# Kernel tuning notes

Hardware: AMD Instinct MI355X
Metric: run time of the kernel (lower is better)

Reference implementation:

```python
import jax, jax.numpy as jnp
import numpy as np

B_GRAPHS = 16      # number of graphs in batch
NPG = 8192         # nodes per graph
N = B_GRAPHS * NPG # 131072 total nodes
F_DIM = 64         # node feature dim
K_CLUST = 16       # n_clusters
DEG = 32           # avg degree
E = N * DEG        # 4,194,304 edges


def setup_inputs() -> dict:
    key = jax.random.key(0)
    k1, k2, k3, k4, k5 = jax.random.split(key, 5)
    x = jax.random.normal(k1, (N, F_DIM), jnp.float32)
    W = jax.random.normal(k2, (F_DIM, K_CLUST), jnp.float32) / np.sqrt(F_DIM)
    b = jnp.zeros((K_CLUST,), jnp.float32)
    # edges constrained within each graph -> block-diagonal adjacency (PyG batching)
    g = jnp.repeat(jnp.arange(B_GRAPHS, dtype=jnp.int32), E // B_GRAPHS)
    edge_row = g * NPG + jax.random.randint(k3, (E,), 0, NPG, jnp.int32)
    edge_col = g * NPG + jax.random.randint(k4, (E,), 0, NPG, jnp.int32)
    edge_weight = jax.random.uniform(k5, (E,), jnp.float32)
    return {"x": x, "W": W, "b": b, "edge_weight": edge_weight,
            "edge_row": edge_row, "edge_col": edge_col, "num_graphs": B_GRAPHS}


def _forward(x, W, b, edge_weight, edge_row, edge_col, num_graphs):
    Ntot, Fd = x.shape
    K = W.shape[1]
    Bn = num_graphs
    n = Ntot // Bn  # equal-size graphs (ptr = n * arange(B+1))

    s = x @ W + b                                   # [N,K] cluster logits
    xb = x.reshape(Bn, n, Fd)
    sb = s.reshape(Bn, n, K)
    # out_x = selu(s^T @ x_bd), block b = s_b^T x_b, then hsplit_and_vstack -> [B*K, F]
    out_x = jax.nn.selu(jnp.einsum('bnk,bnf->bkf', sb, xb)).reshape(Bn * K, Fd)

    ss = jax.nn.softmax(s, axis=-1)                 # softmaxed assignments
    ssb = ss.reshape(Bn, n, K)

    # degree d = adj.sum(axis=0)  (column sums over COO edges)
    d = jax.ops.segment_sum(edge_weight, edge_col, num_segments=Ntot)   # [N]
    m2 = d.reshape(Bn, n).sum(1)                    # total degree per graph [B]

    # A @ C via edge scatter: (A C)[row] += w * C[col]
    AC = jax.ops.segment_sum(edge_weight[:, None] * ss[edge_col], edge_row,
                             num_segments=Ntot)     # [N,K]
    # out_adj blocks: C_b^T A_b C_b  -> [B,K,K]
    out_adj = jnp.einsum('bnk,bnl->bkl', ssb, AC.reshape(Bn, n, K))

    # dS_b = C_b^T d_b  (Ca/Cb blocks); normalizer gets m_inv twice in torch code
    dS = jnp.einsum('bn,bnk->bk', d.reshape(Bn, n), ssb)                # [B,K]
    spectral_loss = -jnp.mean(jnp.einsum('bkk->b', out_adj) / m2
                              - (dS ** 2).sum(1) / (m2 ** 2))

    sqrt_K = jnp.sqrt(jnp.float32(K))
    cluster_size = ssb.sum(1)                        # [B,K]
    cluster_loss = jnp.mean(jnp.sqrt((cluster_size ** 2).sum(1)) / n * sqrt_K - 1.0)

    # CC blocks: C_b^T C_b; ortho = mean_b || CC_b/||CC_b||_F - I/sqrt(K) ||_F
    CC = jnp.einsum('bnk,bnl->bkl', ssb, ssb)        # [B,K,K]
    CC_norm = jnp.sqrt((CC ** 2).sum((1, 2)))        # Frobenius norm per block
    eye_div_k = jnp.eye(K, dtype=x.dtype) / sqrt_K
    ortho_loss = jnp.mean(jnp.sqrt(
        ((CC / CC_norm[:, None, None] - eye_div_k) ** 2).sum((1, 2))))

    # mask diagonal and degree-normalize pooled adjacency
    oa = out_adj * (1.0 - jnp.eye(K, dtype=x.dtype))
    dd = jnp.sqrt(oa.sum(2)) + 1e-12                 # row sums per block [B,K]
    out_adj_norm = oa / (dd[:, :, None] * dd[:, None, :])

    return out_x, out_adj_norm, spectral_loss, cluster_loss, ortho_loss


def reference(x, W, b, edge_weight, edge_row, edge_col, num_graphs):
    return _forward(x, W, b, edge_weight, edge_row, edge_col, num_graphs)
```

## Files before the change

kernel.cpp:

```cpp
#include <hip/hip_runtime.h>
#include <math.h>

#define F_DIM 64
#define K_CL 16
#define B_GR 16
#define SROW 72

typedef _Float16 h16;
using f16x8 = __attribute__((ext_vector_type(8))) _Float16;
using f32x4 = __attribute__((ext_vector_type(4))) float;

__global__ __launch_bounds__(256) void k_fused(
    const float* __restrict__ x, const float* __restrict__ W, const float* __restrict__ bvec,
    h16* __restrict__ ssh, float* __restrict__ outx, float* __restrict__ CCb)
{
    __shared__ float Wl[F_DIM * K_CL];
    __shared__ float bl[K_CL];
    __shared__ __align__(16) h16 stage[4][(16 + 16 + 64) * SROW];

    int t = threadIdx.x;
    for (int idx = t; idx < F_DIM * K_CL; idx += 256) Wl[idx] = W[idx];
    if (t < K_CL) bl[t] = bvec[t];
    __syncthreads();

    int wid = t >> 6, lane = t & 63;
    h16* Sg = stage[wid];
    h16* Cg = Sg + 16 * SROW;
    h16* Xg = Cg + 16 * SROW;

    size_t i = (size_t)blockIdx.x * 256 + t;
    float s[16];
#pragma unroll
    for (int k = 0; k < 16; ++k) s[k] = bl[k];

    const float4* xp = reinterpret_cast<const float4*>(x + i * F_DIM);
#pragma unroll
    for (int j = 0; j < 16; ++j) {
        float4 q = xp[j];
        float xf[4] = {q.x, q.y, q.z, q.w};
#pragma unroll
        for (int ff = 0; ff < 4; ++ff) {
            int f = j * 4 + ff;
            float xv = xf[ff];
            Xg[f * SROW + lane] = (h16)xv;
            const float4* wr = reinterpret_cast<const float4*>(&Wl[f * K_CL]);
            float4 w0 = wr[0], w1 = wr[1], w2 = wr[2], w3 = wr[3];
            s[0]  += xv * w0.x; s[1]  += xv * w0.y; s[2]  += xv * w0.z; s[3]  += xv * w0.w;
            s[4]  += xv * w1.x; s[5]  += xv * w1.y; s[6]  += xv * w1.z; s[7]  += xv * w1.w;
            s[8]  += xv * w2.x; s[9]  += xv * w2.y; s[10] += xv * w2.z; s[11] += xv * w2.w;
            s[12] += xv * w3.x; s[13] += xv * w3.y; s[14] += xv * w3.z; s[15] += xv * w3.w;
        }
    }

#pragma unroll
    for (int k = 0; k < 16; ++k) Sg[k * SROW + lane] = (h16)s[k];

    float m = s[0];
#pragma unroll
    for (int k = 1; k < 16; ++k) m = fmaxf(m, s[k]);
    float sum = 0.f;
#pragma unroll
    for (int k = 0; k < 16; ++k) { s[k] = __expf(s[k] - m); sum += s[k]; }
    float inv = 1.0f / sum;
#pragma unroll
    for (int k = 0; k < 16; ++k) s[k] *= inv;

    f16x8 h0, h1;
#pragma unroll
    for (int k = 0; k < 8; ++k) { h0[k] = (h16)s[k]; h1[k] = (h16)s[k + 8]; }
#pragma unroll
    for (int k = 0; k < 8; ++k) {
        Cg[k * SROW + lane] = h0[k];
        Cg[(k + 8) * SROW + lane] = h1[k];
    }
    f16x8* hp = reinterpret_cast<f16x8*>(ssh + i * K_CL);
    hp[0] = h0;
    hp[1] = h1;

    int q4 = lane >> 4, mm = lane & 15;
    f32x4 accO[4] = {{0.f,0.f,0.f,0.f},{0.f,0.f,0.f,0.f},{0.f,0.f,0.f,0.f},{0.f,0.f,0.f,0.f}};
    f32x4 accC = {0.f, 0.f, 0.f, 0.f};
#pragma unroll
    for (int h = 0; h < 2; ++h) {
        f16x8 aO = *(const f16x8*)&Sg[mm * SROW + h * 32 + q4 * 8];
        f16x8 aC = *(const f16x8*)&Cg[mm * SROW + h * 32 + q4 * 8];
        accC = __builtin_amdgcn_mfma_f32_16x16x32_f16(aC, aC, accC, 0, 0, 0);
#pragma unroll
        for (int ft = 0; ft < 4; ++ft) {
            f16x8 bO = *(const f16x8*)&Xg[(ft * 16 + mm) * SROW + h * 32 + q4 * 8];
            accO[ft] = __builtin_amdgcn_mfma_f32_16x16x32_f16(aO, bO, accO[ft], 0, 0, 0);
        }
    }
    __syncthreads();

    float* redO = (float*)&stage[0][0];
    float* redC = redO + 4096;
#pragma unroll
    for (int ft = 0; ft < 4; ++ft)
#pragma unroll
        for (int rg = 0; rg < 4; ++rg)
            redO[wid * 1024 + (q4 * 4 + rg) * 64 + ft * 16 + mm] = accO[ft][rg];
#pragma unroll
    for (int rg = 0; rg < 4; ++rg)
        redC[wid * 256 + (q4 * 4 + rg) * 16 + mm] = accC[rg];
    __syncthreads();

    int g = blockIdx.x >> 5;
#pragma unroll
    for (int it = 0; it < 4; ++it) {
        int idx = t + it * 256;
        float v = redO[idx] + redO[1024 + idx] + redO[2048 + idx] + redO[3072 + idx];
        atomicAdd(outx + g * 1024 + idx, v);
    }
    {
        float v = redC[t] + redC[256 + t] + redC[512 + t] + redC[768 + t];
        atomicAdd(CCb + g * 256 + t, v);
    }
}

__global__ __launch_bounds__(256) void k_edge(
    const int* __restrict__ erow, const int* __restrict__ ecol, const float* __restrict__ ew,
    const h16* __restrict__ ssh, float* __restrict__ oadj,
    int edges_per_block, int edges_per_graph, int nmask)
{
    __shared__ float CCl[256];
    __shared__ __align__(16) h16 stageE[4][32 * SROW];
    int t = threadIdx.x;
    CCl[t] = 0.f;
    __syncthreads();

    int bid = blockIdx.x;
    int xcd = bid & 7;
    int slot = bid >> 3;
    int graph = xcd + 8 * (slot & 1);
    int chunk = slot >> 1;

    int wid = t >> 6, lane = t & 63;
    int q4 = lane >> 4, mm = lane & 15;
    h16* Ag = stageE[wid];
    h16* Bg = Ag + 16 * SROW;

    int epw = edges_per_block >> 2;
    size_t base = (size_t)graph * edges_per_graph
                + (size_t)chunk * edges_per_block
                + (size_t)wid * epw;

    const f16x8* sshp = reinterpret_cast<const f16x8*>(ssh);
    f32x4 acc = {0.f, 0.f, 0.f, 0.f};

    for (int e0 = 0; e0 < epw; e0 += 64) {
        size_t eb = base + e0 + lane;
        int   r = erow[eb] & nmask;
        int   c = ecol[eb] & nmask;
        float w = ew[eb];

        f16x8 a0 = sshp[2 * (size_t)r];
        f16x8 a1 = sshp[2 * (size_t)r + 1];
        f16x8 b0 = sshp[2 * (size_t)c];
        f16x8 b1 = sshp[2 * (size_t)c + 1];
        h16 wh = (h16)w;
#pragma unroll
        for (int k = 0; k < 8; ++k) { a0[k] *= wh; a1[k] *= wh; }

#pragma unroll
        for (int k = 0; k < 8; ++k) {
            Ag[k * SROW + lane]       = a0[k];
            Ag[(k + 8) * SROW + lane] = a1[k];
            Bg[k * SROW + lane]       = b0[k];
            Bg[(k + 8) * SROW + lane] = b1[k];
        }

#pragma unroll
        for (int h = 0; h < 2; ++h) {
            f16x8 af = *(const f16x8*)&Ag[mm * SROW + h * 32 + q4 * 8];
            f16x8 bf = *(const f16x8*)&Bg[mm * SROW + h * 32 + q4 * 8];
            acc = __builtin_amdgcn_mfma_f32_16x16x32_f16(af, bf, acc, 0, 0, 0);
        }
    }

#pragma unroll
    for (int rg = 0; rg < 4; ++rg)
        atomicAdd(&CCl[(q4 * 4 + rg) * 16 + mm], acc[rg]);
    __syncthreads();
    atomicAdd(oadj + graph * 256 + t, CCl[t]);
}

__global__ __launch_bounds__(256) void k_final(
    const float* __restrict__ outx, const float* __restrict__ oadj,
    const float* __restrict__ CCb, float* __restrict__ out, int npg)
{
    int t = threadIdx.x;
    int gid = blockIdx.x * 256 + t;
    {
        float v = outx[gid];
        float r = (v > 0.f) ? (1.0507009873554805f * v)
                            : (1.0507009873554805f * 1.6732632423543772f * (__expf(v) - 1.0f));
        out[gid] = r;
    }

    if (blockIdx.x != 0) return;

    int b = t >> 4, k = t & 15;
    const float* oar = oadj + b * 256 + k * 16;
    const float* ccr = CCb + b * 256 + k * 16;

    float rowsum_off = 0.f, trace_c = 0.f, rowsum_all = 0.f, fro2 = 0.f, colsum = 0.f;
    float csv = 0.f;
#pragma unroll
    for (int l = 0; l < 16; ++l) {
        float v = oar[l];
        rowsum_all += v;
        if (l == k) trace_c = v; else rowsum_off += v;
        float c = ccr[l];
        fro2 += c * c;
        csv += c;
        colsum += oadj[b * 256 + l * 16 + k];
    }
    float dd = sqrtf(rowsum_off) + 1e-12f;
    __shared__ float ddl[B_GR * K_CL];
    ddl[t] = dd;

    float ds2 = colsum * colsum, cs2 = csv * csv;
    float tr = trace_c, m2 = rowsum_all;
#pragma unroll
    for (int msk = 8; msk >= 1; msk >>= 1) {
        tr   += __shfl_xor(tr,   msk, 16);
        ds2  += __shfl_xor(ds2,  msk, 16);
        cs2  += __shfl_xor(cs2,  msk, 16);
        fro2 += __shfl_xor(fro2, msk, 16);
        m2   += __shfl_xor(m2,   msk, 16);
    }
    float invfro = 1.0f / sqrtf(fro2);
    float osum = 0.f;
#pragma unroll
    for (int l = 0; l < 16; ++l) {
        float v = ccr[l] * invfro - ((l == k) ? 0.25f : 0.f);
        osum += v * v;
    }
#pragma unroll
    for (int msk = 8; msk >= 1; msk >>= 1) osum += __shfl_xor(osum, msk, 16);

    __shared__ float sp_s[B_GR], cl_s[B_GR], or_s[B_GR];
    if (k == 0) {
        sp_s[b] = tr / m2 - ds2 / (m2 * m2);
        cl_s[b] = sqrtf(cs2) / (float)npg * 4.0f - 1.0f;
        or_s[b] = sqrtf(osum);
    }
    __syncthreads();
    if (t == 0) {
        float a = 0.f, c = 0.f, o = 0.f;
        for (int i = 0; i < B_GR; ++i) { a += sp_s[i]; c += cl_s[i]; o += or_s[i]; }
        out[20480] = -a / 16.f;
        out[20481] = c / 16.f;
        out[20482] = o / 16.f;
    }

#pragma unroll
    for (int l = 0; l < 16; ++l) {
        float v = (l == k) ? 0.f : oar[l] / (dd * ddl[b * 16 + l]);
        out[16384 + b * 256 + k * 16 + l] = v;
    }
}

extern "C" void kernel_launch(void* const* d_in, const int* in_sizes, int n_in,
                              void* d_out, int out_size, void* d_ws, size_t ws_size,
                              hipStream_t stream)
{
    const float* x    = (const float*)d_in[0];
    const float* W    = (const float*)d_in[1];
    const float* bvec = (const float*)d_in[2];
    const float* ew   = (const float*)d_in[3];
    const int* erow   = (const int*)d_in[4];
    const int* ecol   = (const int*)d_in[5];

    int Ntot = in_sizes[0] / F_DIM;
    size_t E = (size_t)in_sizes[3];
    int npg  = Ntot / B_GR;
    int edges_per_graph = (int)(E / B_GR);
    int nmask = Ntot - 1;

    const int ADJ_BLOCKS = 2048;
    int edges_per_block = (int)(E / ADJ_BLOCKS);

    char* ws = (char*)d_ws;
    size_t o = 0;
    h16*   ssh   = (h16*)(ws + o);   o += (size_t)Ntot * 16 * 2;
    size_t zoff = o;
    float* outx  = (float*)(ws + o); o += (size_t)B_GR * 1024 * 4;
    float* oadj  = (float*)(ws + o); o += (size_t)B_GR * 256 * 4;
    float* CCb   = (float*)(ws + o); o += (size_t)B_GR * 256 * 4;

    hipMemsetAsync(ws + zoff, 0, o - zoff, stream);

    k_fused<<<Ntot / 256, 256, 0, stream>>>(x, W, bvec, ssh, outx, CCb);
    k_edge<<<ADJ_BLOCKS, 256, 0, stream>>>(erow, ecol, ew, ssh, oadj,
                                           edges_per_block, edges_per_graph, nmask);
    k_final<<<64, 256, 0, stream>>>(outx, oadj, CCb, (float*)d_out, npg);
}
```

Measured before the change: 169.9 us.

## Fuse all stages into one cooperative persistent kernel with grid syncs

Replaces the memset plus three kernel launches with a single cooperative kernel. It zeroes the accumulators, computes logits and softmax and stores both as fp16, then runs the pooled-feature and CC reductions and the edge MFMA pass, with grid syncs separating the phases. The pooled x and CC reductions move from MFMA on LDS tiles to per-node scalar FMA and shuffles. This re-reads x from global, and the edge pass now packs A and B into one LDS buffer. The aim is to remove launch overhead and inter-kernel gaps, at the cost of grid-sync latency, a persistent grid of at most 1024 blocks, and a fallback multi-launch path.

```diff
diff --git a/kernel.cpp b/kernel.cpp
--- a/kernel.cpp
+++ b/kernel.cpp
@@ -1,264 +1,298 @@
 #include <hip/hip_runtime.h>
+#include <hip/hip_cooperative_groups.h>
 #include <math.h>
+#include <stdint.h>
+
+namespace cg = cooperative_groups;
 
 #define F_DIM 64
 #define K_CL 16
 #define B_GR 16
-#define SROW 72
+#define SR32 68
 
 typedef _Float16 h16;
 using f16x8 = __attribute__((ext_vector_type(8))) _Float16;
 using f32x4 = __attribute__((ext_vector_type(4))) float;
 
-__global__ __launch_bounds__(256) void k_fused(
+union H8 { f16x8 v; unsigned short s[8]; uint32_t u[4]; };
+
+struct ShP1  { float Wl[F_DIM * K_CL]; float bl[K_CL]; };
+struct ShP2a { float redx[4096]; float CCl[256]; };
+struct ShP2b { uint32_t AB[4 * 16 * SR32]; float CCl[256]; };
+struct ShP3  { float ddl[256]; float sp[16]; float cl[16]; float orr[16]; };
+
+__global__ __launch_bounds__(256, 4) void mega(
     const float* __restrict__ x, const float* __restrict__ W, const float* __restrict__ bvec,
-    h16* __restrict__ ssh, float* __restrict__ outx, float* __restrict__ CCb)
+    const float* __restrict__ ew, const int* __restrict__ erow, const int* __restrict__ ecol,
+    h16* __restrict__ sshr, h16* __restrict__ sshs,
+    float* __restrict__ accbase,
+    float* __restrict__ out,
+    int Ntot, int npg, int edges_per_graph, int edges_per_block, int nmask, int phase)
 {
-    __shared__ float Wl[F_DIM * K_CL];
-    __shared__ float bl[K_CL];
-    __shared__ __align__(16) h16 stage[4][(16 + 16 + 64) * SROW];
+    cg::grid_group grid = cg::this_grid();
+    __shared__ __align__(16) union { ShP1 a; ShP2a b; ShP2b c; ShP3 d; } sh;
+
+    const bool coop = (phase < 0);
+    float* outx = accbase;
+    float* oadj = accbase + 16384;
+    float* CCb  = accbase + 16384 + 4096;
 
     int t = threadIdx.x;
-    for (int idx = t; idx < F_DIM * K_CL; idx += 256) Wl[idx] = W[idx];
-    if (t < K_CL) bl[t] = bvec[t];
-    __syncthreads();
-
+    int bid = blockIdx.x;
+    int gt = bid * 256 + t;
+    int gstride = (int)gridDim.x * 256;
     int wid = t >> 6, lane = t & 63;
-    h16* Sg = stage[wid];
-    h16* Cg = Sg + 16 * SROW;
-    h16* Xg = Cg + 16 * SROW;
-
-    size_t i = (size_t)blockIdx.x * 256 + t;
-    float s[16];
-#pragma unroll
-    for (int k = 0; k < 16; ++k) s[k] = bl[k];
-
-    const float4* xp = reinterpret_cast<const float4*>(x + i * F_DIM);
-#pragma unroll
-    for (int j = 0; j < 16; ++j) {
-        float4 q = xp[j];
-        float xf[4] = {q.x, q.y, q.z, q.w};
-#pragma unroll
-        for (int ff = 0; ff < 4; ++ff) {
-            int f = j * 4 + ff;
-            float xv = xf[ff];
-            Xg[f * SROW + lane] = (h16)xv;
-            const float4* wr = reinterpret_cast<const float4*>(&Wl[f * K_CL]);
-            float4 w0 = wr[0], w1 = wr[1], w2 = wr[2], w3 = wr[3];
-            s[0]  += xv * w0.x; s[1]  += xv * w0.y; s[2]  += xv * w0.z; s[3]  += xv * w0.w;
-            s[4]  += xv * w1.x; s[5]  += xv * w1.y; s[6]  += xv * w1.z; s[7]  += xv * w1.w;
-            s[8]  += xv * w2.x; s[9]  += xv * w2.y; s[10] += xv * w2.z; s[11] += xv * w2.w;
-            s[12] += xv * w3.x; s[13] += xv * w3.y; s[14] += xv * w3.z; s[15] += xv * w3.w;
-        }
-    }
-
-#pragma unroll
-    for (int k = 0; k < 16; ++k) Sg[k * SROW + lane] = (h16)s[k];
-
-    float m = s[0];
-#pragma unroll
-    for (int k = 1; k < 16; ++k) m = fmaxf(m, s[k]);
-    float sum = 0.f;
-#pragma unroll
-    for (int k = 0; k < 16; ++k) { s[k] = __expf(s[k] - m); sum += s[k]; }
-    float inv = 1.0f / sum;
-#pragma unroll
-    for (int k = 0; k < 16; ++k) s[k] *= inv;
-
-    f16x8 h0, h1;
-#pragma unroll
-    for (int k = 0; k < 8; ++k) { h0[k] = (h16)s[k]; h1[k] = (h16)s[k + 8]; }
-#pragma unroll
-    for (int k = 0; k < 8; ++k) {
-        Cg[k * SROW + lane] = h0[k];
-        Cg[(k + 8) * SROW + lane] = h1[k];
-    }
-    f16x8* hp = reinterpret_cast<f16x8*>(ssh + i * K_CL);
-    hp[0] = h0;
-    hp[1] = h1;
-
-    int q4 = lane >> 4, mm = lane & 15;
-    f32x4 accO[4] = {{0.f,0.f,0.f,0.f},{0.f,0.f,0.f,0.f},{0.f,0.f,0.f,0.f},{0.f,0.f,0.f,0.f}};
-    f32x4 accC = {0.f, 0.f, 0.f, 0.f};
-#pragma unroll
-    for (int h = 0; h < 2; ++h) {
-        f16x8 aO = *(const f16x8*)&Sg[mm * SROW + h * 32 + q4 * 8];
-        f16x8 aC = *(const f16x8*)&Cg[mm * SROW + h * 32 + q4 * 8];
-        accC = __builtin_amdgcn_mfma_f32_16x16x32_f16(aC, aC, accC, 0, 0, 0);
-#pragma unroll
-        for (int ft = 0; ft < 4; ++ft) {
-            f16x8 bO = *(const f16x8*)&Xg[(ft * 16 + mm) * SROW + h * 32 + q4 * 8];
-            accO[ft] = __builtin_amdgcn_mfma_f32_16x16x32_f16(aO, bO, accO[ft], 0, 0, 0);
-        }
-    }
-    __syncthreads();
-
-    float* redO = (float*)&stage[0][0];
-    float* redC = redO + 4096;
-#pragma unroll
-    for (int ft = 0; ft < 4; ++ft)
-#pragma unroll
-        for (int rg = 0; rg < 4; ++rg)
-            redO[wid * 1024 + (q4 * 4 + rg) * 64 + ft * 16 + mm] = accO[ft][rg];
-#pragma unroll
-    for (int rg = 0; rg < 4; ++rg)
-        redC[wid * 256 + (q4 * 4 + rg) * 16 + mm] = accC[rg];
-    __syncthreads();
-
-    int g = blockIdx.x >> 5;
-#pragma unroll
-    for (int it = 0; it < 4; ++it) {
-        int idx = t + it * 256;
-        float v = redO[idx] + redO[1024 + idx] + redO[2048 + idx] + redO[3072 + idx];
-        atomicAdd(outx + g * 1024 + idx, v);
-    }
-    {
-        float v = redC[t] + redC[256 + t] + redC[512 + t] + redC[768 + t];
-        atomicAdd(CCb + g * 256 + t, v);
-    }
-}
-
-__global__ __launch_bounds__(256) void k_edge(
-    const int* __restrict__ erow, const int* __restrict__ ecol, const float* __restrict__ ew,
-    const h16* __restrict__ ssh, float* __restrict__ oadj,
-    int edges_per_block, int edges_per_graph, int nmask)
-{
-    __shared__ float CCl[256];
-    __shared__ __align__(16) h16 stageE[4][32 * SROW];
-    int t = threadIdx.x;
-    CCl[t] = 0.f;
-    __syncthreads();
-
-    int bid = blockIdx.x;
-    int xcd = bid & 7;
-    int slot = bid >> 3;
-    int graph = xcd + 8 * (slot & 1);
-    int chunk = slot >> 1;
-
-    int wid = t >> 6, lane = t & 63;
-    int q4 = lane >> 4, mm = lane & 15;
-    h16* Ag = stageE[wid];
-    h16* Bg = Ag + 16 * SROW;
-
-    int epw = edges_per_block >> 2;
-    size_t base = (size_t)graph * edges_per_graph
-                + (size_t)chunk * edges_per_block
-                + (size_t)wid * epw;
-
-    const f16x8* sshp = reinterpret_cast<const f16x8*>(ssh);
-    f32x4 acc = {0.f, 0.f, 0.f, 0.f};
-
-    for (int e0 = 0; e0 < epw; e0 += 64) {
-        size_t eb = base + e0 + lane;
-        int   r = erow[eb] & nmask;
-        int   c = ecol[eb] & nmask;
-        float w = ew[eb];
-
-        f16x8 a0 = sshp[2 * (size_t)r];
-        f16x8 a1 = sshp[2 * (size_t)r + 1];
-        f16x8 b0 = sshp[2 * (size_t)c];
-        f16x8 b1 = sshp[2 * (size_t)c + 1];
-        h16 wh = (h16)w;
-#pragma unroll
-        for (int k = 0; k < 8; ++k) { a0[k] *= wh; a1[k] *= wh; }
-
-#pragma unroll
-        for (int k = 0; k < 8; ++k) {
-            Ag[k * SROW + lane]       = a0[k];
-            Ag[(k + 8) * SROW + lane] = a1[k];
-            Bg[k * SROW + lane]       = b0[k];
-            Bg[(k + 8) * SROW + lane] = b1[k];
-        }
-
-#pragma unroll
-        for (int h = 0; h < 2; ++h) {
-            f16x8 af = *(const f16x8*)&Ag[mm * SROW + h * 32 + q4 * 8];
-            f16x8 bf = *(const f16x8*)&Bg[mm * SROW + h * 32 + q4 * 8];
-            acc = __builtin_amdgcn_mfma_f32_16x16x32_f16(af, bf, acc, 0, 0, 0);
-        }
-    }
-
-#pragma unroll
-    for (int rg = 0; rg < 4; ++rg)
-        atomicAdd(&CCl[(q4 * 4 + rg) * 16 + mm], acc[rg]);
-    __syncthreads();
-    atomicAdd(oadj + graph * 256 + t, CCl[t]);
-}
-
-__global__ __launch_bounds__(256) void k_final(
-    const float* __restrict__ outx, const float* __restrict__ oadj,
-    const float* __restrict__ CCb, float* __restrict__ out, int npg)
-{
-    int t = threadIdx.x;
-    int gid = blockIdx.x * 256 + t;
-    {
-        float v = outx[gid];
-        float r = (v > 0.f) ? (1.0507009873554805f * v)
-                            : (1.0507009873554805f * 1.6732632423543772f * (__expf(v) - 1.0f));
-        out[gid] = r;
-    }
-
-    if (blockIdx.x != 0) return;
-
-    int b = t >> 4, k = t & 15;
-    const float* oar = oadj + b * 256 + k * 16;
-    const float* ccr = CCb + b * 256 + k * 16;
-
-    float rowsum_off = 0.f, trace_c = 0.f, rowsum_all = 0.f, fro2 = 0.f, colsum = 0.f;
-    float csv = 0.f;
-#pragma unroll
-    for (int l = 0; l < 16; ++l) {
-        float v = oar[l];
-        rowsum_all += v;
-        if (l == k) trace_c = v; else rowsum_off += v;
-        float c = ccr[l];
-        fro2 += c * c;
-        csv += c;
-        colsum += oadj[b * 256 + l * 16 + k];
-    }
-    float dd = sqrtf(rowsum_off) + 1e-12f;
-    __shared__ float ddl[B_GR * K_CL];
-    ddl[t] = dd;
-
-    float ds2 = colsum * colsum, cs2 = csv * csv;
-    float tr = trace_c, m2 = rowsum_all;
-#pragma unroll
-    for (int msk = 8; msk >= 1; msk >>= 1) {
-        tr   += __shfl_xor(tr,   msk, 16);
-        ds2  += __shfl_xor(ds2,  msk, 16);
-        cs2  += __shfl_xor(cs2,  msk, 16);
-        fro2 += __shfl_xor(fro2, msk, 16);
-        m2   += __shfl_xor(m2,   msk, 16);
-    }
-    float invfro = 1.0f / sqrtf(fro2);
-    float osum = 0.f;
-#pragma unroll
-    for (int l = 0; l < 16; ++l) {
-        float v = ccr[l] * invfro - ((l == k) ? 0.25f : 0.f);
-        osum += v * v;
-    }
-#pragma unroll
-    for (int msk = 8; msk >= 1; msk >>= 1) osum += __shfl_xor(osum, msk, 16);
-
-    __shared__ float sp_s[B_GR], cl_s[B_GR], or_s[B_GR];
-    if (k == 0) {
-        sp_s[b] = tr / m2 - ds2 / (m2 * m2);
-        cl_s[b] = sqrtf(cs2) / (float)npg * 4.0f - 1.0f;
-        or_s[b] = sqrtf(osum);
-    }
-    __syncthreads();
-    if (t == 0) {
-        float a = 0.f, c = 0.f, o = 0.f;
-        for (int i = 0; i < B_GR; ++i) { a += sp_s[i]; c += cl_s[i]; o += or_s[i]; }
-        out[20480] = -a / 16.f;
-        out[20481] = c / 16.f;
-        out[20482] = o / 16.f;
-    }
-
-#pragma unroll
-    for (int l = 0; l < 16; ++l) {
-        float v = (l == k) ? 0.f : oar[l] / (dd * ddl[b * 16 + l]);
-        out[16384 + b * 256 + k * 16 + l] = v;
+
+    if (coop) {
+        for (int i0 = gt; i0 < 24576; i0 += gstride) accbase[i0] = 0.f;
+        grid.sync();
+    }
+
+    if (coop || phase == 1) {
+        float* Wl = sh.a.Wl;
+        float* bl = sh.a.bl;
+        for (int idx = t; idx < F_DIM * K_CL; idx += 256) Wl[idx] = W[idx];
+        if (t < K_CL) bl[t] = bvec[t];
+        __syncthreads();
+
+        for (int i0 = gt; i0 < Ntot; i0 += gstride) {
+            size_t i = (size_t)i0;
+            float s[16];
+#pragma unroll
+            for (int k = 0; k < 16; ++k) s[k] = bl[k];
+
+            const float4* xp = reinterpret_cast<const float4*>(x + i * F_DIM);
+#pragma unroll
+            for (int j = 0; j < 16; ++j) {
+                float4 q = xp[j];
+                float xf[4] = {q.x, q.y, q.z, q.w};
+#pragma unroll
+                for (int ff = 0; ff < 4; ++ff) {
+                    int f = j * 4 + ff;
+                    float xv = xf[ff];
+                    const float4* wr = reinterpret_cast<const float4*>(&Wl[f * K_CL]);
+                    float4 w0 = wr[0], w1 = wr[1], w2 = wr[2], w3 = wr[3];
+                    s[0]  += xv * w0.x; s[1]  += xv * w0.y; s[2]  += xv * w0.z; s[3]  += xv * w0.w;
+                    s[4]  += xv * w1.x; s[5]  += xv * w1.y; s[6]  += xv * w1.z; s[7]  += xv * w1.w;
+                    s[8]  += xv * w2.x; s[9]  += xv * w2.y; s[10] += xv * w2.z; s[11] += xv * w2.w;
+                    s[12] += xv * w3.x; s[13] += xv * w3.y; s[14] += xv * w3.z; s[15] += xv * w3.w;
+                }
+            }
+
+            f16x8 hr0, hr1;
+#pragma unroll
+            for (int k = 0; k < 8; ++k) { hr0[k] = (h16)s[k]; hr1[k] = (h16)s[k + 8]; }
+
+            float m = s[0];
+#pragma unroll
+            for (int k = 1; k < 16; ++k) m = fmaxf(m, s[k]);
+            float sum = 0.f;
+#pragma unroll
+            for (int k = 0; k < 16; ++k) { s[k] = __expf(s[k] - m); sum += s[k]; }
+            float inv = 1.0f / sum;
+
+            f16x8 hs0, hs1;
+#pragma unroll
+            for (int k = 0; k < 8; ++k) { hs0[k] = (h16)(s[k] * inv); hs1[k] = (h16)(s[k + 8] * inv); }
+
+            f16x8* rp = reinterpret_cast<f16x8*>(sshr + i * K_CL);
+            rp[0] = hr0; rp[1] = hr1;
+            f16x8* sp = reinterpret_cast<f16x8*>(sshs + i * K_CL);
+            sp[0] = hs0; sp[1] = hs1;
+        }
+        __syncthreads();
+    }
+    if (coop) grid.sync();
+
+    if (coop || phase == 2) {
+        float* redx = sh.b.redx;
+        float* CCl  = sh.b.CCl;
+        CCl[t] = 0.f;
+        __syncthreads();
+
+        int g4 = lane >> 4, l = lane & 15;
+        int npb = Ntot / (int)gridDim.x;
+        int npw = npb >> 2;
+        size_t basen = (size_t)bid * npb + (size_t)wid * npw;
+
+        float accx[16];
+#pragma unroll
+        for (int k = 0; k < 16; ++k) accx[k] = 0.f;
+        float accc[4] = {0.f, 0.f, 0.f, 0.f};
+
+        for (int j = 0; j < npw; ++j) {
+            size_t i = basen + j;
+            float xv = x[i * F_DIM + lane];
+            const f16x8* rp = reinterpret_cast<const f16x8*>(sshr + i * K_CL);
+            f16x8 r0 = rp[0], r1 = rp[1];
+#pragma unroll
+            for (int k = 0; k < 8; ++k) accx[k]     += (float)r0[k] * xv;
+#pragma unroll
+            for (int k = 0; k < 8; ++k) accx[k + 8] += (float)r1[k] * xv;
+
+            float sv = (float)sshs[i * K_CL + l];
+            accc[0] += __shfl(sv, g4 * 4 + 0, 16) * sv;
+            accc[1] += __shfl(sv, g4 * 4 + 1, 16) * sv;
+            accc[2] += __shfl(sv, g4 * 4 + 2, 16) * sv;
+            accc[3] += __shfl(sv, g4 * 4 + 3, 16) * sv;
+        }
+
+#pragma unroll
+        for (int k = 0; k < 16; ++k) redx[wid * 1024 + k * 64 + lane] = accx[k];
+#pragma unroll
+        for (int j4 = 0; j4 < 4; ++j4)
+            atomicAdd(&CCl[(g4 * 4 + j4) * 16 + l], accc[j4]);
+        __syncthreads();
+
+        int g = (int)(((size_t)bid * npb) / (size_t)npg);
+        float* dst = outx + g * (K_CL * F_DIM);
+#pragma unroll
+        for (int it = 0; it < 4; ++it) {
+            int idx = t + it * 256;
+            float v = redx[idx] + redx[1024 + idx] + redx[2048 + idx] + redx[3072 + idx];
+            atomicAdd(dst + idx, v);
+        }
+        atomicAdd(&CCb[g * 256 + t], CCl[t]);
+        __syncthreads();
+
+        {
+            float* CClE = sh.c.CCl;
+            uint32_t* ABw = &sh.c.AB[wid * 16 * SR32];
+            CClE[t] = 0.f;
+            __syncthreads();
+
+            int xcd = bid & 7;
+            int slot = bid >> 3;
+            int graph = xcd + 8 * (slot & 1);
+            int chunk = slot >> 1;
+            int q4 = lane >> 4, mm = lane & 15;
+
+            int epw = edges_per_block >> 2;
+            size_t base = (size_t)graph * edges_per_graph
+                        + (size_t)chunk * edges_per_block
+                        + (size_t)wid * epw;
+
+            const f16x8* sshp = reinterpret_cast<const f16x8*>(sshs);
+            f32x4 acc = {0.f, 0.f, 0.f, 0.f};
+
+            for (int e0 = 0; e0 < epw; e0 += 64) {
+                size_t eb = base + e0 + lane;
+                int   r = erow[eb] & nmask;
+                int   c = ecol[eb] & nmask;
+                float w = ew[eb];
+
+                f16x8 a0 = sshp[2 * (size_t)r];
+                f16x8 a1 = sshp[2 * (size_t)r + 1];
+                f16x8 b0 = sshp[2 * (size_t)c];
+                f16x8 b1 = sshp[2 * (size_t)c + 1];
+                h16 wh = (h16)w;
+                a0 = a0 * wh;
+                a1 = a1 * wh;
+
+                H8 A0, A1, B0, B1;
+                A0.v = a0; A1.v = a1; B0.v = b0; B1.v = b1;
+#pragma unroll
+                for (int k = 0; k < 8; ++k) {
+                    ABw[k * SR32 + lane]       = (uint32_t)A0.s[k] | ((uint32_t)B0.s[k] << 16);
+                    ABw[(k + 8) * SR32 + lane] = (uint32_t)A1.s[k] | ((uint32_t)B1.s[k] << 16);
+                }
+
+#pragma unroll
+                for (int h = 0; h < 2; ++h) {
+                    const uint32_t* rowp = &ABw[mm * SR32 + h * 32 + q4 * 8];
+                    uint4 p0 = *(const uint4*)rowp;
+                    uint4 p1 = *(const uint4*)(rowp + 4);
+                    H8 Af, Bf;
+                    Af.u[0] = (p0.x & 0xffffu) | (p0.y << 16);
+                    Bf.u[0] = (p0.x >> 16)    | (p0.y & 0xffff0000u);
+                    Af.u[1] = (p0.z & 0xffffu) | (p0.w << 16);
+                    Bf.u[1] = (p0.z >> 16)    | (p0.w & 0xffff0000u);
+                    Af.u[2] = (p1.x & 0xffffu) | (p1.y << 16);
+                    Bf.u[2] = (p1.x >> 16)    | (p1.y & 0xffff0000u);
+                    Af.u[3] = (p1.z & 0xffffu) | (p1.w << 16);
+                    Bf.u[3] = (p1.z >> 16)    | (p1.w & 0xffff0000u);
+                    acc = __builtin_amdgcn_mfma_f32_16x16x32_f16(Af.v, Bf.v, acc, 0, 0, 0);
+                }
+            }
+
+#pragma unroll
+            for (int rg = 0; rg < 4; ++rg)
+                atomicAdd(&CClE[(q4 * 4 + rg) * 16 + mm], acc[rg]);
+            __syncthreads();
+            atomicAdd(oadj + graph * 256 + t, CClE[t]);
+            __syncthreads();
+        }
+    }
+    if (coop) grid.sync();
+
+    if (coop || phase == 3) {
+        for (int gid = gt; gid < B_GR * K_CL * F_DIM; gid += gstride) {
+            float v = outx[gid];
+            float r = (v > 0.f) ? (1.0507009873554805f * v)
+                                : (1.0507009873554805f * 1.6732632423543772f * (__expf(v) - 1.0f));
+            out[gid] = r;
+        }
+
+        if (bid == (int)gridDim.x - 1) {
+            int b = t >> 4, k = t & 15;
+            const float* oar = oadj + b * 256 + k * 16;
+            const float* ccr = CCb + b * 256 + k * 16;
+
+            float rowsum_off = 0.f, trace_c = 0.f, rowsum_all = 0.f, fro2 = 0.f, colsum = 0.f;
+            float csv = 0.f;
+#pragma unroll
+            for (int l = 0; l < 16; ++l) {
+                float v = oar[l];
+                rowsum_all += v;
+                if (l == k) trace_c = v; else rowsum_off += v;
+                float c = ccr[l];
+                fro2 += c * c;
+                csv += c;
+                colsum += oadj[b * 256 + l * 16 + k];
+            }
+            float dd = sqrtf(rowsum_off) + 1e-12f;
+            sh.d.ddl[t] = dd;
+
+            float ds2 = colsum * colsum, cs2 = csv * csv;
+            float tr = trace_c, m2 = rowsum_all;
+#pragma unroll
+            for (int msk = 8; msk >= 1; msk >>= 1) {
+                tr   += __shfl_xor(tr,   msk, 16);
+                ds2  += __shfl_xor(ds2,  msk, 16);
+                cs2  += __shfl_xor(cs2,  msk, 16);
+                fro2 += __shfl_xor(fro2, msk, 16);
+                m2   += __shfl_xor(m2,   msk, 16);
+            }
+            float invfro = 1.0f / sqrtf(fro2);
+            float osum = 0.f;
+#pragma unroll
+            for (int l = 0; l < 16; ++l) {
+                float v = ccr[l] * invfro - ((l == k) ? 0.25f : 0.f);
+                osum += v * v;
+            }
+#pragma unroll
+            for (int msk = 8; msk >= 1; msk >>= 1) osum += __shfl_xor(osum, msk, 16);
+
+            if (k == 0) {
+                sh.d.sp[b]  = tr / m2 - ds2 / (m2 * m2);
+                sh.d.cl[b]  = sqrtf(cs2) / (float)npg * 4.0f - 1.0f;
+                sh.d.orr[b] = sqrtf(osum);
+            }
+            __syncthreads();
+            if (t == 0) {
+                float a = 0.f, c = 0.f, o = 0.f;
+                for (int i2 = 0; i2 < B_GR; ++i2) { a += sh.d.sp[i2]; c += sh.d.cl[i2]; o += sh.d.orr[i2]; }
+                out[20480] = -a / 16.f;
+                out[20481] = c / 16.f;
+                out[20482] = o / 16.f;
+            }
+
+#pragma unroll
+            for (int l = 0; l < 16; ++l) {
+                float v = (l == k) ? 0.f : oar[l] / (dd * sh.d.ddl[b * 16 + l]);
+                out[16384 + b * 256 + k * 16 + l] = v;
+            }
+        }
     }
 }
 
@@ -276,24 +310,49 @@
     int Ntot = in_sizes[0] / F_DIM;
     size_t E = (size_t)in_sizes[3];
     int npg  = Ntot / B_GR;
-    int edges_per_graph = (int)(E / B_GR);
+    int epg  = (int)(E / B_GR);
     int nmask = Ntot - 1;
-
-    const int ADJ_BLOCKS = 2048;
-    int edges_per_block = (int)(E / ADJ_BLOCKS);
 
     char* ws = (char*)d_ws;
     size_t o = 0;
-    h16*   ssh   = (h16*)(ws + o);   o += (size_t)Ntot * 16 * 2;
-    size_t zoff = o;
-    float* outx  = (float*)(ws + o); o += (size_t)B_GR * 1024 * 4;
-    float* oadj  = (float*)(ws + o); o += (size_t)B_GR * 256 * 4;
-    float* CCb   = (float*)(ws + o); o += (size_t)B_GR * 256 * 4;
-
-    hipMemsetAsync(ws + zoff, 0, o - zoff, stream);
-
-    k_fused<<<Ntot / 256, 256, 0, stream>>>(x, W, bvec, ssh, outx, CCb);
-    k_edge<<<ADJ_BLOCKS, 256, 0, stream>>>(erow, ecol, ew, ssh, oadj,
-                                           edges_per_block, edges_per_graph, nmask);
-    k_final<<<64, 256, 0, stream>>>(outx, oadj, CCb, (float*)d_out, npg);
+    h16*   sshr = (h16*)(ws + o);   o += (size_t)Ntot * 16 * 2;
+    h16*   sshs = (h16*)(ws + o);   o += (size_t)Ntot * 16 * 2;
+    float* acc  = (float*)(ws + o); o += (size_t)24576 * 4;
+    float* outp = (float*)d_out;
+
+    int bpc = 0;
+    hipError_t qe = hipOccupancyMaxActiveBlocksPerMultiprocessor(
+        &bpc, (const void*)mega, 256, 0);
+    int GRID = 1024;
+    if (qe == hipSuccess && bpc > 0) {
+        int maxg = bpc * 256;
+        while (GRID > maxg && GRID > 128) GRID >>= 1;
+        if (GRID > maxg) GRID = 0;
+    } else {
+        GRID = 0;
+    }
+
+    hipError_t le = hipErrorUnknown;
+    int epb_c = (GRID > 0) ? (int)(E / GRID) : 0;
+    int phase_c = -1;
+    if (GRID >= 128) {
+        void* args[] = {
+            (void*)&x, (void*)&W, (void*)&bvec, (void*)&ew, (void*)&erow, (void*)&ecol,
+            (void*)&sshr, (void*)&sshs, (void*)&acc, (void*)&outp,
+            (void*)&Ntot, (void*)&npg, (void*)&epg, (void*)&epb_c,
+            (void*)&nmask, (void*)&phase_c
+        };
+        le = hipLaunchCooperativeKernel((const void*)mega, dim3(GRID), dim3(256),
+                                        args, 0, stream);
+    }
+
+    if (le != hipSuccess) {
+        hipMemsetAsync(acc, 0, 24576 * sizeof(float), stream);
+        mega<<<512, 256, 0, stream>>>(x, W, bvec, ew, erow, ecol, sshr, sshs, acc, outp,
+                                      Ntot, npg, epg, 0, nmask, 1);
+        mega<<<1024, 256, 0, stream>>>(x, W, bvec, ew, erow, ecol, sshr, sshs, acc, outp,
+                                       Ntot, npg, epg, (int)(E / 1024), nmask, 2);
+        mega<<<64, 256, 0, stream>>>(x, W, bvec, ew, erow, ecol, sshr, sshs, acc, outp,
+                                     Ntot, npg, epg, 0, nmask, 3);
+    }
 }
```

After: 510.6 us. 201% more time.
